# Kernel tuning notes

Hardware: AMD Instinct MI355X
Metric: run time of the kernel (lower is better)

The kernel has to match this reference:

```python
import jax, jax.numpy as jnp
import numpy as np

WS = 8
HEADS = 12


def _dwconv(x, w, b):
    # x: (N, C, H, W); w: (C, 1, 3, 3) depthwise, zero pad 1
    y = jax.lax.conv_general_dilated(
        x, w, window_strides=(1, 1), padding=((1, 1), (1, 1)),
        dimension_numbers=("NCHW", "OIHW", "NCHW"), feature_group_count=x.shape[1])
    return y + b[None, :, None, None]


def _sepconv(x, dw, db, pw, pb):
    y = _dwconv(x, dw, db)
    # pointwise 1x1 conv: (N,C,H,W) x (O,C) -> (N,O,H,W)
    return jnp.einsum("nchw,oc->nohw", y, pw) + pb[None, :, None, None]


def _rel_pos_index(ws):
    coords = np.stack(np.meshgrid(np.arange(ws), np.arange(ws), indexing="ij"))  # (2, ws, ws)
    cf = coords.reshape(2, -1)
    rel = cf[:, :, None] - cf[:, None, :]          # (2, ws*ws, ws*ws)
    rel = rel.transpose(1, 2, 0).copy()
    rel[..., 0] += ws - 1
    rel[..., 1] += ws - 1
    rel[..., 0] *= 2 * ws - 1
    return rel.sum(-1)                             # (ws*ws, ws*ws)


def setup_inputs() -> dict:
    key = jax.random.key(0)
    ks = jax.random.split(key, 16)
    B, T, C, H, W = 2, 1, 384, 192, 192
    s = 0.02
    inp = {
        "vid": jax.random.normal(ks[0], (B, T, C, H, W), jnp.float32),
        "qd_w": jax.random.normal(ks[1], (C, 1, 3, 3), jnp.float32) * s,
        "qd_b": jnp.zeros((C,), jnp.float32),
        "qp_w": jax.random.normal(ks[2], (C, C), jnp.float32) * s,
        "qp_b": jnp.zeros((C,), jnp.float32),
        "kd_w": jax.random.normal(ks[3], (C, 1, 3, 3), jnp.float32) * s,
        "kd_b": jnp.zeros((C,), jnp.float32),
        "kp_w": jax.random.normal(ks[4], (C, C), jnp.float32) * s,
        "kp_b": jnp.zeros((C,), jnp.float32),
        "vd_w": jax.random.normal(ks[5], (C, 1, 3, 3), jnp.float32) * s,
        "vd_b": jnp.zeros((C,), jnp.float32),
        "vp_w": jax.random.normal(ks[6], (C, C), jnp.float32) * s,
        "vp_b": jnp.zeros((C,), jnp.float32),
        "rpb_table": jax.random.normal(ks[7], ((2 * WS - 1) ** 2, HEADS), jnp.float32) * s,
        "proj_w": jax.random.normal(ks[8], (C, C), jnp.float32) * s,
        "proj_b": jnp.zeros((C,), jnp.float32),
    }
    return inp


def reference(vid, qd_w, qd_b, qp_w, qp_b, kd_w, kd_b, kp_w, kp_b,
              vd_w, vd_b, vp_w, vp_b, rpb_table, proj_w, proj_b):
    B, T, C, H, W = vid.shape
    heads, ws = HEADS, WS
    hd = C // heads
    scale = hd ** -0.5
    x = vid.reshape(B * T, C, H, W)

    q = _sepconv(x, qd_w, qd_b, qp_w, qp_b) * scale
    k = _sepconv(x, kd_w, kd_b, kp_w, kp_b)
    v = _sepconv(x, vd_w, vd_b, vp_w, vp_b)

    nh, nw = H // ws, W // ws

    def win(z):  # (N, C, H, W) -> (N*nh*nw, heads, ws*ws, hd)
        N = z.shape[0]
        z = z.reshape(N, heads, hd, nh, ws, nw, ws)
        z = z.transpose(0, 3, 5, 1, 4, 6, 2)  # N, nh, nw, heads, ws, ws, hd
        return z.reshape(N * nh * nw, heads, ws * ws, hd)

    qw, kw, vw = win(q), win(k), win(v)

    # product search within window (dists = q . k), rel-pos bias softmax
    attn = jnp.einsum("nhqd,nhkd->nhqk", qw, kw)
    rp_idx = _rel_pos_index(ws)  # static (64, 64)
    bias = rpb_table[rp_idx.reshape(-1)].reshape(ws * ws, ws * ws, heads)
    bias = bias.transpose(2, 0, 1)  # (heads, 64, 64)
    attn = jax.nn.softmax(attn + bias[None], axis=-1)

    # weighted patch sum (ps=1 -> pixels)
    out = jnp.einsum("nhqk,nhkd->nhqd", attn, vw)  # (N*nh*nw, heads, ws*ws, hd)

    # un-window, merge heads into (h c) channel order, then token projection
    out = out.reshape(B * T, nh, nw, heads, ws, ws, hd)
    out = out.transpose(0, 1, 4, 2, 5, 3, 6).reshape(B * T, H, W, heads * hd)
    out = out @ proj_w.T + proj_b

    # fold (ps=1, stride0=1): identity overlap-add, zvid == 1
    out = out.transpose(0, 3, 1, 2).reshape(B, T, C, H, W)
    return out
```

## Files before the change

### kernel.cpp

```cpp
#include <hip/hip_runtime.h>

#define CCH 384
#define HH 192
#define WWD 192
#define NIMG 2
#define HWP (HH * WWD)
#define PTOT (NIMG * HWP)
#define HEADS 12
#define HD 32
#define NWIN 24
#define WINS 576
#define EELEM ((size_t)NIMG * CCH * HWP)
#define WMAT 147456

typedef __attribute__((ext_vector_type(8))) short bh8;
typedef __attribute__((ext_vector_type(8))) unsigned short us8;
typedef __attribute__((ext_vector_type(4))) unsigned short us4;
typedef __attribute__((ext_vector_type(4))) float fx4;

__device__ __forceinline__ unsigned short f2bf(float f) {
    unsigned u = __float_as_uint(f);
    u += 0x7fffu + ((u >> 16) & 1u);
    return (unsigned short)(u >> 16);
}

__global__ __launch_bounds__(256) void wcvt(
    const float* __restrict__ a, const float* __restrict__ b,
    const float* __restrict__ c, const float* __restrict__ d,
    unsigned short* __restrict__ o)
{
    int idx8 = (blockIdx.x * 256 + threadIdx.x) * 8;
    int which = idx8 / WMAT;
    int loc = idx8 - which * WMAT;
    const float* s = (which == 0) ? a : (which == 1) ? b : (which == 2) ? c : d;
    float4 v0 = *(const float4*)(s + loc);
    float4 v1 = *(const float4*)(s + loc + 4);
    us8 ov;
    ov[0] = f2bf(v0.x); ov[1] = f2bf(v0.y); ov[2] = f2bf(v0.z); ov[3] = f2bf(v0.w);
    ov[4] = f2bf(v1.x); ov[5] = f2bf(v1.y); ov[6] = f2bf(v1.z); ov[7] = f2bf(v1.w);
    *(us8*)(o + idx8) = ov;
}

__global__ __launch_bounds__(256) void dwgather(
    const float* __restrict__ x,
    const float* __restrict__ qw, const float* __restrict__ qb,
    const float* __restrict__ kw, const float* __restrict__ kb,
    const float* __restrict__ vw, const float* __restrict__ vb,
    unsigned short* __restrict__ oq, unsigned short* __restrict__ ok,
    unsigned short* __restrict__ ov)
{
    __shared__ float halo[64 * 11 * 17];

    int widx = blockIdx.x;
    int n = widx / WINS, wrem = widx - n * WINS;
    int wy = wrem / NWIN, wx = wrem - wy * NWIN;
    int h0 = wy * 8, w0 = wx * 8;
    int tid = threadIdx.x;
    int c = tid & 63, pxg = tid >> 6;

    const float* xn = x + (size_t)n * CCH * HWP;

    for (int cb = 0; cb < 6; ++cb) {
        int cg = cb * 64 + c;
        float wq[9], wk[9], wv[9];
#pragma unroll
        for (int t = 0; t < 9; ++t) {
            wq[t] = qw[cg * 9 + t];
            wk[t] = kw[cg * 9 + t];
            wv[t] = vw[cg * 9 + t];
        }
        float bqv = qb[cg], bkv = kb[cg], bvv = vb[cg];

        __syncthreads();
#pragma unroll
        for (int it = 0; it < 10; ++it) {
            int job = it * 256 + tid;
            int seg = job & 3;
            int r   = (job >> 2) % 10;
            int cc  = job / 40;
            int hr  = h0 - 1 + r;
            bool okr = (hr >= 0) && (hr < HH);
            bool okc = !((wx == 0 && seg == 0) || (wx == NWIN - 1 && seg == 3));
            float4 val;
            if (okr && okc)
                val = *(const float4*)(xn + (size_t)(cb * 64 + cc) * HWP
                                          + (size_t)hr * WWD + (w0 - 4) + seg * 4);
            else
                val = make_float4(0.f, 0.f, 0.f, 0.f);
            int bidx = (cc * 11 + r) * 17 + seg * 4;
            halo[bidx + 0] = val.x;
            halo[bidx + 1] = val.y;
            halo[bidx + 2] = val.z;
            halo[bidx + 3] = val.w;
        }
        __syncthreads();

#pragma unroll
        for (int i = 0; i < 16; ++i) {
            int px = pxg * 16 + i;
            int pr = px >> 3, pc = px & 7;
            float sq = 0.f, sk = 0.f, sv = 0.f;
#pragma unroll
            for (int dr = 0; dr < 3; ++dr)
#pragma unroll
                for (int dc = 0; dc < 3; ++dc) {
                    float xv = halo[(c * 11 + pr + dr) * 17 + pc + dc + 3];
                    int t = dr * 3 + dc;
                    sq = fmaf(xv, wq[t], sq);
                    sk = fmaf(xv, wk[t], sk);
                    sv = fmaf(xv, wv[t], sv);
                }
            size_t ob = ((size_t)widx * 64 + px) * CCH + cg;
            oq[ob] = f2bf(sq + bqv);
            ok[ob] = f2bf(sk + bkv);
            ov[ob] = f2bf(sv + bvv);
        }
    }
}

template<int ORIENT>
__global__ __launch_bounds__(256) void pw_gemm(
    const unsigned short* __restrict__ Y, const unsigned short* __restrict__ Wb,
    const float* __restrict__ bias, float scale,
    unsigned short* __restrict__ outb, float* __restrict__ outf)
{
    __shared__ unsigned short Wt[128][40];
    __shared__ unsigned short Yt[128][40];

    int tid = threadIdx.x;
    int pp0 = blockIdx.x * 128;
    int cm0 = blockIdx.y * 128;
    int lid = tid & 63, wid = tid >> 6;
    int wr = wid >> 1, wc = wid & 1;
    int li = lid & 15, g = lid >> 4;
    int srow = tid >> 2;
    int skoff = (tid & 3) * 8;

    fx4 acc[4][4];
#pragma unroll
    for (int i = 0; i < 4; ++i)
#pragma unroll
        for (int j = 0; j < 4; ++j) acc[i][j] = (fx4){0.f, 0.f, 0.f, 0.f};

    const unsigned short* WpG = Wb + (size_t)(cm0 + srow) * CCH + skoff;
    const unsigned short* YpG = Y  + (size_t)(pp0 + srow) * CCH + skoff;
    bh8 w0 = *(const bh8*)(WpG);
    bh8 w1 = *(const bh8*)(WpG + (size_t)64 * CCH);
    bh8 y0 = *(const bh8*)(YpG);
    bh8 y1 = *(const bh8*)(YpG + (size_t)64 * CCH);

    typedef unsigned short (*tile_t)[40];
    tile_t Asrc = (ORIENT == 1) ? Wt : Yt;
    tile_t Bsrc = (ORIENT == 1) ? Yt : Wt;

    for (int kt = 0; kt < 12; ++kt) {
        __syncthreads();
        *(bh8*)&Wt[srow][skoff]      = w0;
        *(bh8*)&Wt[64 + srow][skoff] = w1;
        *(bh8*)&Yt[srow][skoff]      = y0;
        *(bh8*)&Yt[64 + srow][skoff] = y1;
        __syncthreads();
        if (kt < 11) {
            int ko = (kt + 1) * 32;
            w0 = *(const bh8*)(WpG + ko);
            w1 = *(const bh8*)(WpG + ko + (size_t)64 * CCH);
            y0 = *(const bh8*)(YpG + ko);
            y1 = *(const bh8*)(YpG + ko + (size_t)64 * CCH);
        }
        bh8 a[4], b[4];
#pragma unroll
        for (int mf = 0; mf < 4; ++mf)
            a[mf] = *(const bh8*)&Asrc[wr * 64 + mf * 16 + li][g * 8];
#pragma unroll
        for (int nf = 0; nf < 4; ++nf)
            b[nf] = *(const bh8*)&Bsrc[wc * 64 + nf * 16 + li][g * 8];
#pragma unroll
        for (int mf = 0; mf < 4; ++mf)
#pragma unroll
            for (int nf = 0; nf < 4; ++nf)
                acc[mf][nf] = __builtin_amdgcn_mfma_f32_16x16x32_bf16(
                    a[mf], b[nf], acc[mf][nf], 0, 0, 0);
    }

    if (ORIENT == 1) {
#pragma unroll
        for (int mf = 0; mf < 4; ++mf) {
            int c = cm0 + wr * 64 + mf * 16 + g * 4;
            float4 bv = *(const float4*)&bias[c];
#pragma unroll
            for (int nf = 0; nf < 4; ++nf) {
                int p = pp0 + wc * 64 + nf * 16 + li;
                us4 o;
                o[0] = f2bf((acc[mf][nf][0] + bv.x) * scale);
                o[1] = f2bf((acc[mf][nf][1] + bv.y) * scale);
                o[2] = f2bf((acc[mf][nf][2] + bv.z) * scale);
                o[3] = f2bf((acc[mf][nf][3] + bv.w) * scale);
                *(us4*)(outb + (size_t)p * CCH + c) = o;
            }
        }
    } else if (ORIENT == 2) {
#pragma unroll
        for (int nf = 0; nf < 4; ++nf) {
            int c = cm0 + wc * 64 + nf * 16 + li;
            float bv = bias[c];
#pragma unroll
            for (int mf = 0; mf < 4; ++mf) {
                int p = pp0 + wr * 64 + mf * 16 + g * 4;
                int n = p / HWP;
                int pl = p - n * HWP;
                us4 o;
                o[0] = f2bf(acc[mf][nf][0] + bv);
                o[1] = f2bf(acc[mf][nf][1] + bv);
                o[2] = f2bf(acc[mf][nf][2] + bv);
                o[3] = f2bf(acc[mf][nf][3] + bv);
                *(us4*)(outb + (size_t)(n * CCH + c) * HWP + pl) = o;
            }
        }
    } else {
#pragma unroll
        for (int nf = 0; nf < 4; ++nf) {
            int c = cm0 + wc * 64 + nf * 16 + li;
            float bv = bias[c];
#pragma unroll
            for (int mf = 0; mf < 4; ++mf) {
                int p = pp0 + wr * 64 + mf * 16 + g * 4;
                int n = p / HWP;
                int rem = p - n * HWP;
                int win = rem >> 6, t = rem & 63;
                int h = (win / NWIN) * 8 + (t >> 3);
                int w = (win % NWIN) * 8 + (t & 7);
                float4 o;
                o.x = acc[mf][nf][0] + bv;
                o.y = acc[mf][nf][1] + bv;
                o.z = acc[mf][nf][2] + bv;
                o.w = acc[mf][nf][3] + bv;
                *(float4*)(outf + (size_t)(n * CCH + c) * HWP + h * WWD + w) = o;
            }
        }
    }
}

__global__ __launch_bounds__(256) void attn(
    const unsigned short* __restrict__ q, const unsigned short* __restrict__ k,
    const unsigned short* __restrict__ v, const float* __restrict__ rpb,
    unsigned short* __restrict__ o)
{
    __shared__ float rpbs[225 * HEADS];
    __shared__ unsigned short Pl[4][64][72];

    int tid = threadIdx.x, lid = tid & 63, wid = tid >> 6;
    int wl = blockIdx.x;
    int n = wl / WINS, winl = wl - n * WINS;
    int li = lid & 15, g = lid >> 4;

    for (int i = tid; i < 225 * HEADS; i += 256) rpbs[i] = rpb[i];
    __syncthreads();

    const fx4 z = (fx4){0.f, 0.f, 0.f, 0.f};

    for (int hq = wid; hq < HEADS; hq += 4) {
        const unsigned short* qp = q + (size_t)(wl * 64) * CCH + hq * HD + g * 8;
        const unsigned short* kp = k + (size_t)(wl * 64) * CCH + hq * HD + g * 8;
        bh8 aq[4], bk[4];
#pragma unroll
        for (int mf = 0; mf < 4; ++mf)
            aq[mf] = *(const bh8*)(qp + (size_t)(mf * 16 + li) * CCH);
#pragma unroll
        for (int nf = 0; nf < 4; ++nf)
            bk[nf] = *(const bh8*)(kp + (size_t)(nf * 16 + li) * CCH);

        fx4 s[4][4];
#pragma unroll
        for (int mf = 0; mf < 4; ++mf)
#pragma unroll
            for (int nf = 0; nf < 4; ++nf)
                s[mf][nf] = __builtin_amdgcn_mfma_f32_16x16x32_bf16(aq[mf], bk[nf], z, 0, 0, 0);

#pragma unroll
        for (int mf = 0; mf < 4; ++mf)
#pragma unroll
            for (int nf = 0; nf < 4; ++nf)
#pragma unroll
                for (int r = 0; r < 4; ++r) {
                    int tq = mf * 16 + g * 4 + r, tk = nf * 16 + li;
                    int dy = (tq >> 3) - (tk >> 3) + 7;
                    int dx = (tq & 7) - (tk & 7) + 7;
                    s[mf][nf][r] += rpbs[(dy * 15 + dx) * HEADS + hq];
                }

        float inv_[4][4];
#pragma unroll
        for (int mf = 0; mf < 4; ++mf)
#pragma unroll
            for (int r = 0; r < 4; ++r) {
                float m = s[mf][0][r];
#pragma unroll
                for (int nf = 1; nf < 4; ++nf) m = fmaxf(m, s[mf][nf][r]);
                m = fmaxf(m, __shfl_xor(m, 1));
                m = fmaxf(m, __shfl_xor(m, 2));
                m = fmaxf(m, __shfl_xor(m, 4));
                m = fmaxf(m, __shfl_xor(m, 8));
                float sum = 0.f;
#pragma unroll
                for (int nf = 0; nf < 4; ++nf) {
                    float e = __expf(s[mf][nf][r] - m);
                    s[mf][nf][r] = e;
                    sum += e;
                }
                sum += __shfl_xor(sum, 1);
                sum += __shfl_xor(sum, 2);
                sum += __shfl_xor(sum, 4);
                sum += __shfl_xor(sum, 8);
                inv_[mf][r] = 1.f / sum;
            }

#pragma unroll
        for (int mf = 0; mf < 4; ++mf)
#pragma unroll
            for (int nf = 0; nf < 4; ++nf)
#pragma unroll
                for (int r = 0; r < 4; ++r)
                    Pl[wid][mf * 16 + g * 4 + r][nf * 16 + li] =
                        f2bf(s[mf][nf][r] * inv_[mf][r]);

        fx4 o2[2][4];
#pragma unroll
        for (int m2 = 0; m2 < 2; ++m2)
#pragma unroll
            for (int nf = 0; nf < 4; ++nf) o2[m2][nf] = z;
#pragma unroll
        for (int ks = 0; ks < 2; ++ks) {
            bh8 av[2], bp[4];
#pragma unroll
            for (int m2 = 0; m2 < 2; ++m2)
                av[m2] = *(const bh8*)(v + (size_t)(n * CCH + hq * HD + m2 * 16 + li) * HWP
                                         + winl * 64 + ks * 32 + g * 8);
#pragma unroll
            for (int nf = 0; nf < 4; ++nf)
                bp[nf] = *(const bh8*)&Pl[wid][nf * 16 + li][ks * 32 + g * 8];
#pragma unroll
            for (int m2 = 0; m2 < 2; ++m2)
#pragma unroll
                for (int nf = 0; nf < 4; ++nf)
                    o2[m2][nf] = __builtin_amdgcn_mfma_f32_16x16x32_bf16(
                        av[m2], bp[nf], o2[m2][nf], 0, 0, 0);
        }
#pragma unroll
        for (int nf = 0; nf < 4; ++nf) {
            int tq = nf * 16 + li;
#pragma unroll
            for (int m2 = 0; m2 < 2; ++m2) {
                int d = hq * HD + m2 * 16 + g * 4;
                us4 ov;
                ov[0] = f2bf(o2[m2][nf][0]);
                ov[1] = f2bf(o2[m2][nf][1]);
                ov[2] = f2bf(o2[m2][nf][2]);
                ov[3] = f2bf(o2[m2][nf][3]);
                *(us4*)(o + (size_t)(wl * 64 + tq) * CCH + d) = ov;
            }
        }
    }
}

extern "C" void kernel_launch(void* const* d_in, const int* in_sizes, int n_in,
                              void* d_out, int out_size, void* d_ws, size_t ws_size,
                              hipStream_t stream) {
    const float* vid  = (const float*)d_in[0];
    const float* qd_w = (const float*)d_in[1];
    const float* qd_b = (const float*)d_in[2];
    const float* qp_w = (const float*)d_in[3];
    const float* qp_b = (const float*)d_in[4];
    const float* kd_w = (const float*)d_in[5];
    const float* kd_b = (const float*)d_in[6];
    const float* kp_w = (const float*)d_in[7];
    const float* kp_b = (const float*)d_in[8];
    const float* vd_w = (const float*)d_in[9];
    const float* vd_b = (const float*)d_in[10];
    const float* vp_w = (const float*)d_in[11];
    const float* vp_b = (const float*)d_in[12];
    const float* rpb  = (const float*)d_in[13];
    const float* pj_w = (const float*)d_in[14];
    const float* pj_b = (const float*)d_in[15];

    unsigned short* ws16 = (unsigned short*)d_ws;
    unsigned short* tr0 = ws16 + 3 * EELEM;
    unsigned short* tr1 = ws16 + 4 * EELEM;
    unsigned short* tr2 = ws16 + 5 * EELEM;
    unsigned short* Wb  = ws16 + 6 * EELEM;
    unsigned short* qb  = ws16;
    unsigned short* kb  = ws16 + EELEM;
    unsigned short* vb  = ws16 + 2 * EELEM;
    unsigned short* ob  = tr0;

    wcvt<<<288, 256, 0, stream>>>(qp_w, kp_w, vp_w, pj_w, Wb);
    dwgather<<<NIMG * WINS, 256, 0, stream>>>(
        vid, qd_w, qd_b, kd_w, kd_b, vd_w, vd_b, tr0, tr1, tr2);

    dim3 gg(PTOT / 128, 3);
    const float scale = 0.17677669529663687f;
    pw_gemm<1><<<gg, 256, 0, stream>>>(tr0, Wb,             qp_b, scale, qb, nullptr);
    pw_gemm<1><<<gg, 256, 0, stream>>>(tr1, Wb + WMAT,      kp_b, 1.0f,  kb, nullptr);
    pw_gemm<2><<<gg, 256, 0, stream>>>(tr2, Wb + 2 * WMAT,  vp_b, 1.0f,  vb, nullptr);

    attn<<<NIMG * WINS, 256, 0, stream>>>(qb, kb, vb, rpb, ob);

    pw_gemm<3><<<gg, 256, 0, stream>>>(ob, Wb + 3 * WMAT, pj_b, 1.0f, nullptr, (float*)d_out);
}
```

Measured before the change: 429.6 us.

## Restructure depthwise gather to per-pixel threads with vectorized channel stores

The depthwise conv+gather kernel now assigns each thread one pixel across a 4-window-wide tile and loops over 16 channels per chunk, instead of one channel per thread over 16 pixels. Outputs are packed into 8-wide bf16 vectors and written as contiguous 16-byte stores along the channel dimension, replacing scattered 2-byte stores. Halo loads use float4 shared-memory writes, and blocks are swizzled across channel groups. Weights are now read from global (uniform, likely scalar loads) per channel, which may add load latency but frees registers.

```diff
diff --git a/kernel.cpp b/kernel.cpp
--- a/kernel.cpp
+++ b/kernel.cpp
@@ -49,72 +49,72 @@
     unsigned short* __restrict__ oq, unsigned short* __restrict__ ok,
     unsigned short* __restrict__ ov)
 {
-    __shared__ float halo[64 * 11 * 17];
-
-    int widx = blockIdx.x;
-    int n = widx / WINS, wrem = widx - n * WINS;
-    int wy = wrem / NWIN, wx = wrem - wy * NWIN;
-    int h0 = wy * 8, w0 = wx * 8;
+    __shared__ float halo[16 * 10 * 40];
+
+    int bid = blockIdx.x;
+    int b = (bid & 7) * 144 + (bid >> 3);
+    int cgroup = b & 3;
+    int tile = b >> 2;
+    int n = tile / 144;
+    int trem = tile - n * 144;
+    int wy = trem / 6, wtx = trem - wy * 6;
+
     int tid = threadIdx.x;
-    int c = tid & 63, pxg = tid >> 6;
+    int r8 = tid >> 5;
+    int c32 = tid & 31;
+    int wloc = c32 >> 3;
+    int pxw = r8 * 8 + (c32 & 7);
+    int widx = n * WINS + wy * NWIN + wtx * 4 + wloc;
+    size_t outbase = ((size_t)widx * 64 + pxw) * CCH;
 
     const float* xn = x + (size_t)n * CCH * HWP;
-
-    for (int cb = 0; cb < 6; ++cb) {
-        int cg = cb * 64 + c;
-        float wq[9], wk[9], wv[9];
-#pragma unroll
-        for (int t = 0; t < 9; ++t) {
-            wq[t] = qw[cg * 9 + t];
-            wk[t] = kw[cg * 9 + t];
-            wv[t] = vw[cg * 9 + t];
-        }
-        float bqv = qb[cg], bkv = kb[cg], bvv = vb[cg];
+    int h0 = wy * 8;
+    int col0 = wtx * 32 - 4;
+
+    for (int ch = 0; ch < 6; ++ch) {
+        int cg0 = cgroup * 96 + ch * 16;
 
         __syncthreads();
-#pragma unroll
-        for (int it = 0; it < 10; ++it) {
-            int job = it * 256 + tid;
-            int seg = job & 3;
-            int r   = (job >> 2) % 10;
-            int cc  = job / 40;
-            int hr  = h0 - 1 + r;
-            bool okr = (hr >= 0) && (hr < HH);
-            bool okc = !((wx == 0 && seg == 0) || (wx == NWIN - 1 && seg == 3));
-            float4 val;
-            if (okr && okc)
-                val = *(const float4*)(xn + (size_t)(cb * 64 + cc) * HWP
-                                          + (size_t)hr * WWD + (w0 - 4) + seg * 4);
-            else
-                val = make_float4(0.f, 0.f, 0.f, 0.f);
-            int bidx = (cc * 11 + r) * 17 + seg * 4;
-            halo[bidx + 0] = val.x;
-            halo[bidx + 1] = val.y;
-            halo[bidx + 2] = val.z;
-            halo[bidx + 3] = val.w;
+        for (int job = tid; job < 1600; job += 256) {
+            int seg = job % 10;
+            int rr  = (job / 10) % 10;
+            int cc  = job / 100;
+            int hr  = h0 - 1 + rr;
+            int cb  = col0 + seg * 4;
+            float4 val = make_float4(0.f, 0.f, 0.f, 0.f);
+            if (hr >= 0 && hr < HH && cb >= 0 && cb < WWD)
+                val = *(const float4*)(xn + (size_t)(cg0 + cc) * HWP
+                                          + (size_t)hr * WWD + cb);
+            *(float4*)&halo[(cc * 10 + rr) * 40 + seg * 4] = val;
         }
         __syncthreads();
 
-#pragma unroll
-        for (int i = 0; i < 16; ++i) {
-            int px = pxg * 16 + i;
-            int pr = px >> 3, pc = px & 7;
+        us8 oqv[2], okv[2], ovv[2];
+#pragma unroll
+        for (int j = 0; j < 16; ++j) {
+            int cg = cg0 + j;
             float sq = 0.f, sk = 0.f, sv = 0.f;
 #pragma unroll
-            for (int dr = 0; dr < 3; ++dr)
+            for (int dr = 0; dr < 3; ++dr) {
 #pragma unroll
                 for (int dc = 0; dc < 3; ++dc) {
-                    float xv = halo[(c * 11 + pr + dr) * 17 + pc + dc + 3];
+                    float xv = halo[(j * 10 + r8 + dr) * 40 + c32 + dc + 3];
                     int t = dr * 3 + dc;
-                    sq = fmaf(xv, wq[t], sq);
-                    sk = fmaf(xv, wk[t], sk);
-                    sv = fmaf(xv, wv[t], sv);
+                    sq = fmaf(xv, qw[cg * 9 + t], sq);
+                    sk = fmaf(xv, kw[cg * 9 + t], sk);
+                    sv = fmaf(xv, vw[cg * 9 + t], sv);
                 }
-            size_t ob = ((size_t)widx * 64 + px) * CCH + cg;
-            oq[ob] = f2bf(sq + bqv);
-            ok[ob] = f2bf(sk + bkv);
-            ov[ob] = f2bf(sv + bvv);
-        }
+            }
+            oqv[j >> 3][j & 7] = f2bf(sq + qb[cg]);
+            okv[j >> 3][j & 7] = f2bf(sk + kb[cg]);
+            ovv[j >> 3][j & 7] = f2bf(sv + vb[cg]);
+        }
+        *(us8*)(oq + outbase + cg0)     = oqv[0];
+        *(us8*)(oq + outbase + cg0 + 8) = oqv[1];
+        *(us8*)(ok + outbase + cg0)     = okv[0];
+        *(us8*)(ok + outbase + cg0 + 8) = okv[1];
+        *(us8*)(ov + outbase + cg0)     = ovv[0];
+        *(us8*)(ov + outbase + cg0 + 8) = ovv[1];
     }
 }
 
```

Result: slower. 518.9 us (+20.8%).

## Split depthwise gather across channel groups with tighter halo and XCD-aware block mapping

Applied to the files above, without the earlier changes.

The depthwise-conv gather kernel now launches one block per (window, 64-channel group) instead of looping over six channel groups inside each block. The halo load reads 12 columns per row instead of 16, with a scalar fallback at image edges. Block IDs are remapped with a modulo-8 swizzle, apparently to spread work across the chip's compute dies. The goals are more parallelism, less shared memory per block for higher occupancy, and less over-fetch, at the cost of more blocks and duplicated weight loads.

```diff
diff --git a/kernel.cpp b/kernel.cpp
--- a/kernel.cpp
+++ b/kernel.cpp
@@ -49,72 +49,82 @@
     unsigned short* __restrict__ oq, unsigned short* __restrict__ ok,
     unsigned short* __restrict__ ov)
 {
-    __shared__ float halo[64 * 11 * 17];
-
-    int widx = blockIdx.x;
-    int n = widx / WINS, wrem = widx - n * WINS;
-    int wy = wrem / NWIN, wx = wrem - wy * NWIN;
-    int h0 = wy * 8, w0 = wx * 8;
+    __shared__ float halo[64 * 121];
+
+    int bid = blockIdx.x;
+    int b = (bid & 7) * 864 + (bid >> 3);
+    int wtx  = b % 24;
+    int strip = b / 24;
+    int chv  = strip % 6;
+    int nwy  = strip / 6;
+    int wy   = nwy % 24;
+    int n    = nwy / 24;
+
+    int h0 = wy * 8, w0 = wtx * 8;
     int tid = threadIdx.x;
-    int c = tid & 63, pxg = tid >> 6;
-
-    const float* xn = x + (size_t)n * CCH * HWP;
-
-    for (int cb = 0; cb < 6; ++cb) {
-        int cg = cb * 64 + c;
-        float wq[9], wk[9], wv[9];
-#pragma unroll
-        for (int t = 0; t < 9; ++t) {
-            wq[t] = qw[cg * 9 + t];
-            wk[t] = kw[cg * 9 + t];
-            wv[t] = vw[cg * 9 + t];
-        }
-        float bqv = qb[cg], bkv = kb[cg], bvv = vb[cg];
-
-        __syncthreads();
-#pragma unroll
-        for (int it = 0; it < 10; ++it) {
-            int job = it * 256 + tid;
-            int seg = job & 3;
-            int r   = (job >> 2) % 10;
-            int cc  = job / 40;
-            int hr  = h0 - 1 + r;
-            bool okr = (hr >= 0) && (hr < HH);
-            bool okc = !((wx == 0 && seg == 0) || (wx == NWIN - 1 && seg == 3));
-            float4 val;
-            if (okr && okc)
-                val = *(const float4*)(xn + (size_t)(cb * 64 + cc) * HWP
-                                          + (size_t)hr * WWD + (w0 - 4) + seg * 4);
-            else
-                val = make_float4(0.f, 0.f, 0.f, 0.f);
-            int bidx = (cc * 11 + r) * 17 + seg * 4;
-            halo[bidx + 0] = val.x;
-            halo[bidx + 1] = val.y;
-            halo[bidx + 2] = val.z;
-            halo[bidx + 3] = val.w;
-        }
-        __syncthreads();
-
-#pragma unroll
-        for (int i = 0; i < 16; ++i) {
-            int px = pxg * 16 + i;
-            int pr = px >> 3, pc = px & 7;
-            float sq = 0.f, sk = 0.f, sv = 0.f;
-#pragma unroll
-            for (int dr = 0; dr < 3; ++dr)
-#pragma unroll
-                for (int dc = 0; dc < 3; ++dc) {
-                    float xv = halo[(c * 11 + pr + dr) * 17 + pc + dc + 3];
-                    int t = dr * 3 + dc;
-                    sq = fmaf(xv, wq[t], sq);
-                    sk = fmaf(xv, wk[t], sk);
-                    sv = fmaf(xv, wv[t], sv);
-                }
-            size_t ob = ((size_t)widx * 64 + px) * CCH + cg;
-            oq[ob] = f2bf(sq + bqv);
-            ok[ob] = f2bf(sk + bkv);
-            ov[ob] = f2bf(sv + bvv);
-        }
+    int c   = tid & 63;
+    int pxg = tid >> 6;
+    int cg  = chv * 64 + c;
+    int widx = n * WINS + wy * NWIN + wtx;
+
+    const float* xbase = x + (size_t)n * CCH * HWP + (size_t)(chv * 64) * HWP;
+
+    for (int j = tid; j < 1920; j += 256) {
+        int seg = j % 3;
+        int t   = j / 3;
+        int rr  = t % 10;
+        int cc  = t / 10;
+        int hr  = h0 - 1 + rr;
+        int cb  = w0 - 2 + seg * 4;
+        float4 val = make_float4(0.f, 0.f, 0.f, 0.f);
+        if (hr >= 0 && hr < HH) {
+            const float* p = xbase + (size_t)cc * HWP + (size_t)hr * WWD;
+            if (cb >= 0 && cb + 4 <= WWD) {
+                val = *(const float4*)(p + cb);
+            } else {
+                if (cb + 0 >= 0 && cb + 0 < WWD) val.x = p[cb + 0];
+                if (cb + 1 >= 0 && cb + 1 < WWD) val.y = p[cb + 1];
+                if (cb + 2 >= 0 && cb + 2 < WWD) val.z = p[cb + 2];
+                if (cb + 3 >= 0 && cb + 3 < WWD) val.w = p[cb + 3];
+            }
+        }
+        int hb = cc * 121 + rr * 12 + seg * 4;
+        halo[hb + 0] = val.x;
+        halo[hb + 1] = val.y;
+        halo[hb + 2] = val.z;
+        halo[hb + 3] = val.w;
+    }
+
+    float wq[9], wk[9], wv[9];
+#pragma unroll
+    for (int t = 0; t < 9; ++t) {
+        wq[t] = qw[cg * 9 + t];
+        wk[t] = kw[cg * 9 + t];
+        wv[t] = vw[cg * 9 + t];
+    }
+    float bqv = qb[cg], bkv = kb[cg], bvv = vb[cg];
+
+    __syncthreads();
+
+#pragma unroll
+    for (int i = 0; i < 16; ++i) {
+        int px = pxg * 16 + i;
+        int pr = px >> 3, pc = px & 7;
+        float sq = 0.f, sk = 0.f, sv = 0.f;
+#pragma unroll
+        for (int dr = 0; dr < 3; ++dr)
+#pragma unroll
+            for (int dc = 0; dc < 3; ++dc) {
+                float xv = halo[c * 121 + (pr + dr) * 12 + pc + dc + 1];
+                int t = dr * 3 + dc;
+                sq = fmaf(xv, wq[t], sq);
+                sk = fmaf(xv, wk[t], sk);
+                sv = fmaf(xv, wv[t], sv);
+            }
+        size_t ob = ((size_t)widx * 64 + px) * CCH + cg;
+        oq[ob] = f2bf(sq + bqv);
+        ok[ob] = f2bf(sk + bkv);
+        ov[ob] = f2bf(sv + bvv);
     }
 }
 
@@ -393,7 +403,7 @@
     unsigned short* ob  = tr0;
 
     wcvt<<<288, 256, 0, stream>>>(qp_w, kp_w, vp_w, pj_w, Wb);
-    dwgather<<<NIMG * WINS, 256, 0, stream>>>(
+    dwgather<<<NIMG * WINS * 6, 256, 0, stream>>>(
         vid, qd_w, qd_b, kd_w, kd_b, vd_w, vd_b, tr0, tr1, tr2);
 
     dim3 gg(PTOT / 128, 3);
```

Measured after the change: 405.4 us. -5.6%, faster.
